# Optimization experiments

Measured on AMD Instinct MI355X. Metric: run time of the kernel, lower is better.

## Reference

```python
import jax, jax.numpy as jnp
import numpy as np

B, N, K = 4, 16384, 32
IN_F, OUT_F = 32, 64


def _dense_params(key, fan_in, fan_out):
    kw, _ = jax.random.split(key)
    lim = np.sqrt(6.0 / (fan_in + fan_out)).astype(np.float32)
    W = jax.random.uniform(kw, (fan_in, fan_out), jnp.float32, -lim, lim)
    b = jnp.zeros((fan_out,), jnp.float32)
    return W, b


def setup_inputs() -> dict:
    key = jax.random.key(0)
    ks = jax.random.split(key, 16)
    points = jax.random.normal(ks[0], (B, N, 3), jnp.float32)
    features = jax.random.normal(ks[1], (B, N, IN_F), jnp.float32)
    density = jax.random.uniform(ks[2], (B, N, 1), jnp.float32)
    neighbor_idx = jax.random.randint(ks[3], (B, N, K), 0, N, jnp.int32)
    pe_w1, pe_b1 = _dense_params(ks[4], 3, 64)
    pe_w2, pe_b2 = _dense_params(ks[5], 64, 64)
    mlp_w1, mlp_b1 = _dense_params(ks[6], IN_F + 64, 128)
    mlp_w2, mlp_b2 = _dense_params(ks[7], 128, OUT_F)
    dw_w1, dw_b1 = _dense_params(ks[8], 1, 64)
    dw_w2, dw_b2 = _dense_params(ks[9], 64, 32)
    dw_w3, dw_b3 = _dense_params(ks[10], 32, 1)
    return dict(points=points, features=features, density=density,
                neighbor_idx=neighbor_idx,
                pe_w1=pe_w1, pe_b1=pe_b1, pe_w2=pe_w2, pe_b2=pe_b2,
                mlp_w1=mlp_w1, mlp_b1=mlp_b1, mlp_w2=mlp_w2, mlp_b2=mlp_b2,
                dw_w1=dw_w1, dw_b1=dw_b1, dw_w2=dw_w2, dw_b2=dw_b2,
                dw_w3=dw_w3, dw_b3=dw_b3)


def _gather(x, idx):
    # x: [B,N,D], idx: [B,N,K] -> [B,N,K,D]
    return jax.vmap(lambda xb, ib: xb[ib])(x, idx)


def reference(points, features, density, neighbor_idx,
              pe_w1, pe_b1, pe_w2, pe_b2,
              mlp_w1, mlp_b1, mlp_w2, mlp_b2,
              dw_w1, dw_b1, dw_w2, dw_b2, dw_w3, dw_b3):
    nb_feat = _gather(features, neighbor_idx)                 # [B,N,K,F]
    rel_pos = _gather(points, neighbor_idx) - points[:, :, None, :]  # [B,N,K,3]
    # positional encoding MLP
    pe = jax.nn.relu(rel_pos @ pe_w1 + pe_b1) @ pe_w2 + pe_b2  # [B,N,K,64]
    cat = jnp.concatenate([nb_feat, pe], axis=-1)              # [B,N,K,F+64]
    h = jax.nn.relu(cat @ mlp_w1 + mlp_b1) @ mlp_w2 + mlp_b2   # [B,N,K,OUT_F]
    # density weight MLP on center density (tiled over K in original)
    cd = density[:, :, None, :]                                # [B,N,1,1]
    w = jax.nn.relu(cd @ dw_w1 + dw_b1)
    w = jax.nn.relu(w @ dw_w2 + dw_b2)
    w = jax.nn.sigmoid(w @ dw_w3 + dw_b3)                      # [B,N,1,1]
    w = jnp.broadcast_to(w, (w.shape[0], w.shape[1], K, 1))    # tile to [B,N,K,1]
    w = jax.nn.softmax(w, axis=2)                              # over neighbors
    return jnp.sum(w * h, axis=2)                              # [B,N,OUT_F]
```

## Files before the change

kernel.cpp:

```cpp
#include <hip/hip_runtime.h>

#define BB   4
#define NN   16384
#define KK   32
#define HID  128
#define OUTF 64

typedef _Float16 f16x8 __attribute__((ext_vector_type(8)));
typedef _Float16 f16x4 __attribute__((ext_vector_type(4)));
typedef _Float16 f16x2 __attribute__((ext_vector_type(2)));
typedef float    f32x4 __attribute__((ext_vector_type(4)));

static __device__ __forceinline__ unsigned short h2u(_Float16 h) {
    union { _Float16 h; unsigned short u; } c; c.h = h; return c.u;
}
static __device__ __forceinline__ _Float16 u2h(unsigned short u) {
    union { _Float16 h; unsigned short u; } c; c.u = u; return c.h;
}

#define PE_HALF(T, RX, RY, RZ)                                              \
    (__builtin_shufflevector((T), (T), 6, 7)                                \
     + __builtin_shufflevector((T), (T), 0, 1) * (RX)                       \
     + __builtin_shufflevector((T), (T), 2, 3) * (RY)                       \
     + __builtin_shufflevector((T), (T), 4, 5) * (RZ))

#define PE_FRAGS(E, O1, O2)                                                 \
    do {                                                                    \
        _Float16 _hx = u2h((E).x), _hy = u2h((E).y), _hz = u2h((E).z);      \
        f16x2 _rx = { _hx, _hx }, _ry = { _hy, _hy }, _rz = { _hz, _hz };   \
        f16x2 _z = { (_Float16)0.f, (_Float16)0.f };                        \
        f16x2 _a0 = __builtin_elementwise_max(PE_HALF(tab1[0], _rx, _ry, _rz), _z); \
        f16x2 _a1 = __builtin_elementwise_max(PE_HALF(tab1[1], _rx, _ry, _rz), _z); \
        f16x2 _a2 = __builtin_elementwise_max(PE_HALF(tab1[2], _rx, _ry, _rz), _z); \
        f16x2 _a3 = __builtin_elementwise_max(PE_HALF(tab1[3], _rx, _ry, _rz), _z); \
        f16x2 _b0 = __builtin_elementwise_max(PE_HALF(tab2[0], _rx, _ry, _rz), _z); \
        f16x2 _b1 = __builtin_elementwise_max(PE_HALF(tab2[1], _rx, _ry, _rz), _z); \
        f16x2 _b2 = __builtin_elementwise_max(PE_HALF(tab2[2], _rx, _ry, _rz), _z); \
        f16x2 _b3 = __builtin_elementwise_max(PE_HALF(tab2[3], _rx, _ry, _rz), _z); \
        f16x4 _al = __builtin_shufflevector(_a0, _a1, 0, 1, 2, 3);          \
        f16x4 _ah = __builtin_shufflevector(_a2, _a3, 0, 1, 2, 3);          \
        f16x4 _bl = __builtin_shufflevector(_b0, _b1, 0, 1, 2, 3);          \
        f16x4 _bh = __builtin_shufflevector(_b2, _b3, 0, 1, 2, 3);          \
        O1 = __builtin_shufflevector(_al, _ah, 0, 1, 2, 3, 4, 5, 6, 7);     \
        O2 = __builtin_shufflevector(_bl, _bh, 0, 1, 2, 3, 4, 5, 6, 7);     \
    } while (0)

__global__ __launch_bounds__(256) void prep_all(
    const float* __restrict__ pe_w2, const float* __restrict__ pe_b2,
    const float* __restrict__ mlp_w1, const float* __restrict__ mlp_b1,
    const float* __restrict__ mlp_w2,
    const float* __restrict__ features, const float* __restrict__ points,
    _Float16* __restrict__ gB1, _Float16* __restrict__ gW2,
    float* __restrict__ b1c,
    _Float16* __restrict__ feat16, float4* __restrict__ pts4)
{
    const int bid = blockIdx.x, tid = threadIdx.x;
    if (bid >= 40) {
        if (bid == 2344) {
            if (tid < HID) {
                float a = mlp_b1[tid];
#pragma unroll 16
                for (int c = 0; c < 64; ++c)
                    a = fmaf(pe_b2[c], mlp_w1[(32 + c) * HID + tid], a);
                b1c[tid] = a;
            }
            return;
        }
        int t = (bid - 40) * 256 + tid;
        if (t < BB * NN * 8) {
            float4 v = ((const float4*)features)[t];
            f16x4 h;
            h[0] = (_Float16)v.x; h[1] = (_Float16)v.y;
            h[2] = (_Float16)v.z; h[3] = (_Float16)v.w;
            *(f16x4*)(feat16 + (size_t)t * 4) = h;
        } else {
            int i = t - BB * NN * 8;
            if (i < BB * NN) {
                const float* p = points + (size_t)i * 3;
                pts4[i] = make_float4(p[0], p[1], p[2], 0.f);
            }
        }
        return;
    }
    if (bid < 24) {
        int ks = bid >> 3, nt = bid & 7;
        for (int e = tid; e < 512; e += 256) {
            int l = e >> 3, j = e & 7;
            int k = ks * 32 + (l >> 4) * 8 + j;
            int n = nt * 16 + (l & 15);
            float v;
            if (k < 32) {
                v = mlp_w1[k * HID + n];
            } else {
                int r = k - 32;
                v = 0.f;
#pragma unroll 16
                for (int c = 0; c < 64; ++c)
                    v = fmaf(pe_w2[r * 64 + c], mlp_w1[(32 + c) * HID + n], v);
            }
            gB1[bid * 512 + e] = (_Float16)v;
        }
    } else {
        int tb = bid - 24;
        int ks = tb >> 2, nt = tb & 3;
        for (int e = tid; e < 512; e += 256) {
            int l = e >> 3, j = e & 7;
            int k = ks * 32 + (l >> 4) * 8 + j;
            int n = nt * 16 + (l & 15);
            gW2[tb * 512 + e] = (_Float16)(mlp_w2[k * OUTF + n] * 0.03125f);
        }
    }
}

__global__ __launch_bounds__(512, 4) void DensityAwareFeatureAggregator_main(
    const float4* __restrict__ pts4,
    const _Float16* __restrict__ feat16,
    const int*   __restrict__ nbr,
    const float* __restrict__ pe_w1,
    const float* __restrict__ pe_b1,
    const float* __restrict__ b1c,
    const _Float16* __restrict__ gB1,
    const _Float16* __restrict__ gW2,
    const float* __restrict__ b2g,
    float* __restrict__ out)
{
    __shared__ __align__(16) _Float16 sB1[24 * 512];
    __shared__ __align__(16) f16x8    sTabH[32];
    __shared__ __align__(16) ushort4  sRI[8][64];
    __shared__ __align__(16) _Float16 sHM[8][16 * 136];

    const int t = threadIdx.x;
    {
        const uint4* g = (const uint4*)gB1;
        uint4* d = (uint4*)sB1;
        for (int i = t; i < 1536; i += 512) d[i] = g[i];
    }
    if (t < 32) {
        int cp = t;
        f16x8 e;
        e[0] = (_Float16)pe_w1[2 * cp];       e[1] = (_Float16)pe_w1[2 * cp + 1];
        e[2] = (_Float16)pe_w1[64 + 2 * cp];  e[3] = (_Float16)pe_w1[64 + 2 * cp + 1];
        e[4] = (_Float16)pe_w1[128 + 2 * cp]; e[5] = (_Float16)pe_w1[128 + 2 * cp + 1];
        e[6] = (_Float16)pe_b1[2 * cp];       e[7] = (_Float16)pe_b1[2 * cp + 1];
        sTabH[cp] = e;
    }
    __syncthreads();

    const int w = t >> 6, l = t & 63, q = l >> 4, c16 = l & 15;
    const int nb   = (blockIdx.x & 7) * 64 + (blockIdx.x >> 3);
    const int base = (nb * 8 + w) * 16;
    const int bo   = base & ~(NN - 1);

    f16x8 tab1[4], tab2[4];
#pragma unroll
    for (int u = 0; u < 4; ++u) {
        tab1[u] = sTabH[q * 4 + u];
        tab2[u] = sTabH[16 + q * 4 + u];
    }
    float bias1[8];
#pragma unroll
    for (int nt = 0; nt < 8; ++nt) bias1[nt] = b1c[nt * 16 + c16];

    const f16x8* B1f = (const f16x8*)sB1;
    _Float16* hmw = &sHM[w][0];

#pragma unroll 1
    for (int p2 = 0; p2 < 8; ++p2) {
        const int mA = base + 2 * p2;
        int idx = nbr[(size_t)mA * KK + l];
        float4 pc = pts4[mA + (l >> 5)];
        float4 pn = pts4[bo + idx];
        ushort4 st;
        st.x = h2u((_Float16)(pn.x - pc.x));
        st.y = h2u((_Float16)(pn.y - pc.y));
        st.z = h2u((_Float16)(pn.z - pc.z));
        st.w = (unsigned short)idx;
        sRI[w][l] = st;
        ushort4 eA0 = sRI[w][c16];
        ushort4 eA1 = sRI[w][16 + c16];
        ushort4 eB0 = sRI[w][32 + c16];
        ushort4 eB1 = sRI[w][48 + c16];

        f16x8 afA0 = ((const f16x8*)(feat16 + ((size_t)(bo + eA0.w)) * 32))[q];
        f16x8 afA1 = ((const f16x8*)(feat16 + ((size_t)(bo + eA1.w)) * 32))[q];
        f16x8 afB0 = ((const f16x8*)(feat16 + ((size_t)(bo + eB0.w)) * 32))[q];
        f16x8 afB1 = ((const f16x8*)(feat16 + ((size_t)(bo + eB1.w)) * 32))[q];

        f16x8 apA10, apA20, apA11, apA21, apB10, apB20, apB11, apB21;
        PE_FRAGS(eA0, apA10, apA20);
        PE_FRAGS(eA1, apA11, apA21);
        PE_FRAGS(eB0, apB10, apB20);
        PE_FRAGS(eB1, apB11, apB21);

#pragma unroll 2
        for (int nt = 0; nt < 8; ++nt) {
            f16x8 bf0 = B1f[nt * 64 + l];
            f16x8 bf1 = B1f[(8 + nt) * 64 + l];
            f16x8 bf2 = B1f[(16 + nt) * 64 + l];
            f32x4 aA0, aA1, aB0, aB1;
            aA0[0] = aA0[1] = aA0[2] = aA0[3] = bias1[nt];
            aA1 = aA0; aB0 = aA0; aB1 = aA0;
            aA0 = __builtin_amdgcn_mfma_f32_16x16x32_f16(afA0,  bf0, aA0, 0, 0, 0);
            aA1 = __builtin_amdgcn_mfma_f32_16x16x32_f16(afA1,  bf0, aA1, 0, 0, 0);
            aB0 = __builtin_amdgcn_mfma_f32_16x16x32_f16(afB0,  bf0, aB0, 0, 0, 0);
            aB1 = __builtin_amdgcn_mfma_f32_16x16x32_f16(afB1,  bf0, aB1, 0, 0, 0);
            aA0 = __builtin_amdgcn_mfma_f32_16x16x32_f16(apA10, bf1, aA0, 0, 0, 0);
            aA1 = __builtin_amdgcn_mfma_f32_16x16x32_f16(apA11, bf1, aA1, 0, 0, 0);
            aB0 = __builtin_amdgcn_mfma_f32_16x16x32_f16(apB10, bf1, aB0, 0, 0, 0);
            aB1 = __builtin_amdgcn_mfma_f32_16x16x32_f16(apB11, bf1, aB1, 0, 0, 0);
            aA0 = __builtin_amdgcn_mfma_f32_16x16x32_f16(apA20, bf2, aA0, 0, 0, 0);
            aA1 = __builtin_amdgcn_mfma_f32_16x16x32_f16(apA21, bf2, aA1, 0, 0, 0);
            aB0 = __builtin_amdgcn_mfma_f32_16x16x32_f16(apB20, bf2, aB0, 0, 0, 0);
            aB1 = __builtin_amdgcn_mfma_f32_16x16x32_f16(apB21, bf2, aB1, 0, 0, 0);

            float sA = fmaxf(aA0[0], 0.f) + fmaxf(aA0[1], 0.f)
                     + fmaxf(aA0[2], 0.f) + fmaxf(aA0[3], 0.f)
                     + fmaxf(aA1[0], 0.f) + fmaxf(aA1[1], 0.f)
                     + fmaxf(aA1[2], 0.f) + fmaxf(aA1[3], 0.f);
            float sB = fmaxf(aB0[0], 0.f) + fmaxf(aB0[1], 0.f)
                     + fmaxf(aB0[2], 0.f) + fmaxf(aB0[3], 0.f)
                     + fmaxf(aB1[0], 0.f) + fmaxf(aB1[1], 0.f)
                     + fmaxf(aB1[2], 0.f) + fmaxf(aB1[3], 0.f);
            sA += __shfl_xor(sA, 16, 64);
            sA += __shfl_xor(sA, 32, 64);
            sB += __shfl_xor(sB, 16, 64);
            sB += __shfl_xor(sB, 32, 64);
            if (q == 0) {
                hmw[(2 * p2) * 136 + nt * 16 + c16]     = (_Float16)sA;
                hmw[(2 * p2 + 1) * 136 + nt * 16 + c16] = (_Float16)sB;
            }
        }
    }

    const f16x8* W2f = (const f16x8*)gW2;
    f32x4 acc2[4];
#pragma unroll
    for (int nt = 0; nt < 4; ++nt) {
        f32x4 z; float bv = b2g[nt * 16 + c16];
        z[0] = z[1] = z[2] = z[3] = bv;
        acc2[nt] = z;
    }
#pragma unroll
    for (int ks = 0; ks < 4; ++ks) {
        f16x8 a2 = *(const f16x8*)&hmw[c16 * 136 + ks * 32 + q * 8];
#pragma unroll
        for (int nt = 0; nt < 4; ++nt) {
            f16x8 bf = W2f[(ks * 4 + nt) * 64 + l];
            acc2[nt] = __builtin_amdgcn_mfma_f32_16x16x32_f16(a2, bf, acc2[nt], 0, 0, 0);
        }
    }
#pragma unroll
    for (int nt = 0; nt < 4; ++nt)
#pragma unroll
        for (int r = 0; r < 4; ++r)
            out[(size_t)(base + q * 4 + r) * OUTF + nt * 16 + c16] = acc2[nt][r];
}

extern "C" void kernel_launch(void* const* d_in, const int* in_sizes, int n_in,
                              void* d_out, int out_size, void* d_ws, size_t ws_size,
                              hipStream_t stream)
{
    const float* points   = (const float*)d_in[0];
    const float* features = (const float*)d_in[1];
    const int*   nbr      = (const int*)d_in[3];
    const float* pe_w1    = (const float*)d_in[4];
    const float* pe_b1    = (const float*)d_in[5];
    const float* pe_w2    = (const float*)d_in[6];
    const float* pe_b2    = (const float*)d_in[7];
    const float* mlp_w1   = (const float*)d_in[8];
    const float* mlp_b1   = (const float*)d_in[9];
    const float* mlp_w2   = (const float*)d_in[10];
    const float* mlp_b2   = (const float*)d_in[11];

    float* wsf = (float*)d_ws;
    float*    b1c    = wsf;
    _Float16* gB1    = (_Float16*)(wsf + 128);
    _Float16* gW2    = (_Float16*)(wsf + 6272);
    float4*   pts4   = (float4*)(wsf + 10368);
    _Float16* feat16 = (_Float16*)(wsf + 272512);

    prep_all<<<2345, 256, 0, stream>>>(
        pe_w2, pe_b2, mlp_w1, mlp_b1, mlp_w2, features, points,
        gB1, gW2, b1c, feat16, pts4);

    DensityAwareFeatureAggregator_main<<<512, 512, 0, stream>>>(
        pts4, feat16, nbr, pe_w1, pe_b1, b1c, gB1, gW2, mlp_b2,
        (float*)d_out);
}
```

Before: 173.8 us.

## Precompute packed fp16 relative positions and indices in prep kernel

Moves the neighbor-index load, point gather and relative-position computation from the main kernel into the prep kernel, which writes a packed ushort4 per (point, neighbor) holding the fp16 offsets and the index. The main kernel then reads these records directly, dropping the per-iteration nbr load, point gathers and the shared-memory round trip through sRI. The cost is an extra 2M-entry buffer written and re-read through global memory, plus a much larger prep grid. The old path is kept as a fallback when the workspace is too small.

```diff
diff --git a/kernel.cpp b/kernel.cpp
--- a/kernel.cpp
+++ b/kernel.cpp
@@ -5,6 +5,10 @@
 #define KK   32
 #define HID  128
 #define OUTF 64
+
+#define PREP_WORK_BLOCKS 10240
+#define PREP_GRID        (40 + PREP_WORK_BLOCKS + 1)
+#define PREP_B1C_BID     (40 + PREP_WORK_BLOCKS)
 
 typedef _Float16 f16x8 __attribute__((ext_vector_type(8)));
 typedef _Float16 f16x4 __attribute__((ext_vector_type(4)));
@@ -45,18 +49,19 @@
         O2 = __builtin_shufflevector(_bl, _bh, 0, 1, 2, 3, 4, 5, 6, 7);     \
     } while (0)
 
-__global__ __launch_bounds__(256) void prep_all(
+__global__ __launch_bounds__(256) void prep_v2(
     const float* __restrict__ pe_w2, const float* __restrict__ pe_b2,
     const float* __restrict__ mlp_w1, const float* __restrict__ mlp_b1,
     const float* __restrict__ mlp_w2,
     const float* __restrict__ features, const float* __restrict__ points,
+    const int* __restrict__ nbr,
     _Float16* __restrict__ gB1, _Float16* __restrict__ gW2,
     float* __restrict__ b1c,
-    _Float16* __restrict__ feat16, float4* __restrict__ pts4)
+    _Float16* __restrict__ feat16, ushort4* __restrict__ rel4)
 {
     const int bid = blockIdx.x, tid = threadIdx.x;
     if (bid >= 40) {
-        if (bid == 2344) {
+        if (bid == PREP_B1C_BID) {
             if (tid < HID) {
                 float a = mlp_b1[tid];
 #pragma unroll 16
@@ -67,17 +72,26 @@
             return;
         }
         int t = (bid - 40) * 256 + tid;
-        if (t < BB * NN * 8) {
-            float4 v = ((const float4*)features)[t];
-            f16x4 h;
-            h[0] = (_Float16)v.x; h[1] = (_Float16)v.y;
-            h[2] = (_Float16)v.z; h[3] = (_Float16)v.w;
-            *(f16x4*)(feat16 + (size_t)t * 4) = h;
+        if (t < BB * NN * KK) {
+            int idx = nbr[t];
+            int pt  = t >> 5;
+            int bo  = pt & ~(NN - 1);
+            const float* pc = points + (size_t)pt * 3;
+            const float* pn = points + (size_t)(bo + idx) * 3;
+            ushort4 st;
+            st.x = h2u((_Float16)(pn[0] - pc[0]));
+            st.y = h2u((_Float16)(pn[1] - pc[1]));
+            st.z = h2u((_Float16)(pn[2] - pc[2]));
+            st.w = (unsigned short)idx;
+            rel4[t] = st;
         } else {
-            int i = t - BB * NN * 8;
-            if (i < BB * NN) {
-                const float* p = points + (size_t)i * 3;
-                pts4[i] = make_float4(p[0], p[1], p[2], 0.f);
+            int u = t - BB * NN * KK;
+            if (u < BB * NN * 8) {
+                float4 v = ((const float4*)features)[u];
+                f16x4 h;
+                h[0] = (_Float16)v.x; h[1] = (_Float16)v.y;
+                h[2] = (_Float16)v.z; h[3] = (_Float16)v.w;
+                *(f16x4*)(feat16 + (size_t)u * 4) = h;
             }
         }
         return;
@@ -113,9 +127,8 @@
 }
 
 __global__ __launch_bounds__(512, 4) void DensityAwareFeatureAggregator_main(
-    const float4* __restrict__ pts4,
+    const ushort4* __restrict__ rel4,
     const _Float16* __restrict__ feat16,
-    const int*   __restrict__ nbr,
     const float* __restrict__ pe_w1,
     const float* __restrict__ pe_b1,
     const float* __restrict__ b1c,
@@ -126,7 +139,6 @@
 {
     __shared__ __align__(16) _Float16 sB1[24 * 512];
     __shared__ __align__(16) f16x8    sTabH[32];
-    __shared__ __align__(16) ushort4  sRI[8][64];
     __shared__ __align__(16) _Float16 sHM[8][16 * 136];
 
     const int t = threadIdx.x;
@@ -167,19 +179,11 @@
 #pragma unroll 1
     for (int p2 = 0; p2 < 8; ++p2) {
         const int mA = base + 2 * p2;
-        int idx = nbr[(size_t)mA * KK + l];
-        float4 pc = pts4[mA + (l >> 5)];
-        float4 pn = pts4[bo + idx];
-        ushort4 st;
-        st.x = h2u((_Float16)(pn.x - pc.x));
-        st.y = h2u((_Float16)(pn.y - pc.y));
-        st.z = h2u((_Float16)(pn.z - pc.z));
-        st.w = (unsigned short)idx;
-        sRI[w][l] = st;
-        ushort4 eA0 = sRI[w][c16];
-        ushort4 eA1 = sRI[w][16 + c16];
-        ushort4 eB0 = sRI[w][32 + c16];
-        ushort4 eB1 = sRI[w][48 + c16];
+        const ushort4* rg = rel4 + (size_t)mA * KK;
+        ushort4 eA0 = rg[c16];
+        ushort4 eA1 = rg[16 + c16];
+        ushort4 eB0 = rg[32 + c16];
+        ushort4 eB1 = rg[48 + c16];
 
         f16x8 afA0 = ((const f16x8*)(feat16 + ((size_t)(bo + eA0.w)) * 32))[q];
         f16x8 afA1 = ((const f16x8*)(feat16 + ((size_t)(bo + eA1.w)) * 32))[q];
@@ -256,6 +260,217 @@
             out[(size_t)(base + q * 4 + r) * OUTF + nt * 16 + c16] = acc2[nt][r];
 }
 
+__global__ __launch_bounds__(256) void prep_fb(
+    const float* __restrict__ pe_w2, const float* __restrict__ pe_b2,
+    const float* __restrict__ mlp_w1, const float* __restrict__ mlp_b1,
+    const float* __restrict__ mlp_w2,
+    const float* __restrict__ features, const float* __restrict__ points,
+    _Float16* __restrict__ gB1, _Float16* __restrict__ gW2,
+    float* __restrict__ b1c,
+    _Float16* __restrict__ feat16, float4* __restrict__ pts4)
+{
+    const int bid = blockIdx.x, tid = threadIdx.x;
+    if (bid >= 40) {
+        if (bid == 2344) {
+            if (tid < HID) {
+                float a = mlp_b1[tid];
+#pragma unroll 16
+                for (int c = 0; c < 64; ++c)
+                    a = fmaf(pe_b2[c], mlp_w1[(32 + c) * HID + tid], a);
+                b1c[tid] = a;
+            }
+            return;
+        }
+        int t = (bid - 40) * 256 + tid;
+        if (t < BB * NN * 8) {
+            float4 v = ((const float4*)features)[t];
+            f16x4 h;
+            h[0] = (_Float16)v.x; h[1] = (_Float16)v.y;
+            h[2] = (_Float16)v.z; h[3] = (_Float16)v.w;
+            *(f16x4*)(feat16 + (size_t)t * 4) = h;
+        } else {
+            int i = t - BB * NN * 8;
+            if (i < BB * NN) {
+                const float* p = points + (size_t)i * 3;
+                pts4[i] = make_float4(p[0], p[1], p[2], 0.f);
+            }
+        }
+        return;
+    }
+    if (bid < 24) {
+        int ks = bid >> 3, nt = bid & 7;
+        for (int e = tid; e < 512; e += 256) {
+            int l = e >> 3, j = e & 7;
+            int k = ks * 32 + (l >> 4) * 8 + j;
+            int n = nt * 16 + (l & 15);
+            float v;
+            if (k < 32) {
+                v = mlp_w1[k * HID + n];
+            } else {
+                int r = k - 32;
+                v = 0.f;
+#pragma unroll 16
+                for (int c = 0; c < 64; ++c)
+                    v = fmaf(pe_w2[r * 64 + c], mlp_w1[(32 + c) * HID + n], v);
+            }
+            gB1[bid * 512 + e] = (_Float16)v;
+        }
+    } else {
+        int tb = bid - 24;
+        int ks = tb >> 2, nt = tb & 3;
+        for (int e = tid; e < 512; e += 256) {
+            int l = e >> 3, j = e & 7;
+            int k = ks * 32 + (l >> 4) * 8 + j;
+            int n = nt * 16 + (l & 15);
+            gW2[tb * 512 + e] = (_Float16)(mlp_w2[k * OUTF + n] * 0.03125f);
+        }
+    }
+}
+
+__global__ __launch_bounds__(512, 4) void main_fb(
+    const float4* __restrict__ pts4,
+    const _Float16* __restrict__ feat16,
+    const int*   __restrict__ nbr,
+    const float* __restrict__ pe_w1,
+    const float* __restrict__ pe_b1,
+    const float* __restrict__ b1c,
+    const _Float16* __restrict__ gB1,
+    const _Float16* __restrict__ gW2,
+    const float* __restrict__ b2g,
+    float* __restrict__ out)
+{
+    __shared__ __align__(16) _Float16 sB1[24 * 512];
+    __shared__ __align__(16) f16x8    sTabH[32];
+    __shared__ __align__(16) ushort4  sRI[8][64];
+    __shared__ __align__(16) _Float16 sHM[8][16 * 136];
+
+    const int t = threadIdx.x;
+    {
+        const uint4* g = (const uint4*)gB1;
+        uint4* d = (uint4*)sB1;
+        for (int i = t; i < 1536; i += 512) d[i] = g[i];
+    }
+    if (t < 32) {
+        int cp = t;
+        f16x8 e;
+        e[0] = (_Float16)pe_w1[2 * cp];       e[1] = (_Float16)pe_w1[2 * cp + 1];
+        e[2] = (_Float16)pe_w1[64 + 2 * cp];  e[3] = (_Float16)pe_w1[64 + 2 * cp + 1];
+        e[4] = (_Float16)pe_w1[128 + 2 * cp]; e[5] = (_Float16)pe_w1[128 + 2 * cp + 1];
+        e[6] = (_Float16)pe_b1[2 * cp];       e[7] = (_Float16)pe_b1[2 * cp + 1];
+        sTabH[cp] = e;
+    }
+    __syncthreads();
+
+    const int w = t >> 6, l = t & 63, q = l >> 4, c16 = l & 15;
+    const int nb   = (blockIdx.x & 7) * 64 + (blockIdx.x >> 3);
+    const int base = (nb * 8 + w) * 16;
+    const int bo   = base & ~(NN - 1);
+
+    f16x8 tab1[4], tab2[4];
+#pragma unroll
+    for (int u = 0; u < 4; ++u) {
+        tab1[u] = sTabH[q * 4 + u];
+        tab2[u] = sTabH[16 + q * 4 + u];
+    }
+    float bias1[8];
+#pragma unroll
+    for (int nt = 0; nt < 8; ++nt) bias1[nt] = b1c[nt * 16 + c16];
+
+    const f16x8* B1f = (const f16x8*)sB1;
+    _Float16* hmw = &sHM[w][0];
+
+#pragma unroll 1
+    for (int p2 = 0; p2 < 8; ++p2) {
+        const int mA = base + 2 * p2;
+        int idx = nbr[(size_t)mA * KK + l];
+        float4 pc = pts4[mA + (l >> 5)];
+        float4 pn = pts4[bo + idx];
+        ushort4 st;
+        st.x = h2u((_Float16)(pn.x - pc.x));
+        st.y = h2u((_Float16)(pn.y - pc.y));
+        st.z = h2u((_Float16)(pn.z - pc.z));
+        st.w = (unsigned short)idx;
+        sRI[w][l] = st;
+        ushort4 eA0 = sRI[w][c16];
+        ushort4 eA1 = sRI[w][16 + c16];
+        ushort4 eB0 = sRI[w][32 + c16];
+        ushort4 eB1 = sRI[w][48 + c16];
+
+        f16x8 afA0 = ((const f16x8*)(feat16 + ((size_t)(bo + eA0.w)) * 32))[q];
+        f16x8 afA1 = ((const f16x8*)(feat16 + ((size_t)(bo + eA1.w)) * 32))[q];
+        f16x8 afB0 = ((const f16x8*)(feat16 + ((size_t)(bo + eB0.w)) * 32))[q];
+        f16x8 afB1 = ((const f16x8*)(feat16 + ((size_t)(bo + eB1.w)) * 32))[q];
+
+        f16x8 apA10, apA20, apA11, apA21, apB10, apB20, apB11, apB21;
+        PE_FRAGS(eA0, apA10, apA20);
+        PE_FRAGS(eA1, apA11, apA21);
+        PE_FRAGS(eB0, apB10, apB20);
+        PE_FRAGS(eB1, apB11, apB21);
+
+#pragma unroll 2
+        for (int nt = 0; nt < 8; ++nt) {
+            f16x8 bf0 = B1f[nt * 64 + l];
+            f16x8 bf1 = B1f[(8 + nt) * 64 + l];
+            f16x8 bf2 = B1f[(16 + nt) * 64 + l];
+            f32x4 aA0, aA1, aB0, aB1;
+            aA0[0] = aA0[1] = aA0[2] = aA0[3] = bias1[nt];
+            aA1 = aA0; aB0 = aA0; aB1 = aA0;
+            aA0 = __builtin_amdgcn_mfma_f32_16x16x32_f16(afA0,  bf0, aA0, 0, 0, 0);
+            aA1 = __builtin_amdgcn_mfma_f32_16x16x32_f16(afA1,  bf0, aA1, 0, 0, 0);
+            aB0 = __builtin_amdgcn_mfma_f32_16x16x32_f16(afB0,  bf0, aB0, 0, 0, 0);
+            aB1 = __builtin_amdgcn_mfma_f32_16x16x32_f16(afB1,  bf0, aB1, 0, 0, 0);
+            aA0 = __builtin_amdgcn_mfma_f32_16x16x32_f16(apA10, bf1, aA0, 0, 0, 0);
+            aA1 = __builtin_amdgcn_mfma_f32_16x16x32_f16(apA11, bf1, aA1, 0, 0, 0);
+            aB0 = __builtin_amdgcn_mfma_f32_16x16x32_f16(apB10, bf1, aB0, 0, 0, 0);
+            aB1 = __builtin_amdgcn_mfma_f32_16x16x32_f16(apB11, bf1, aB1, 0, 0, 0);
+            aA0 = __builtin_amdgcn_mfma_f32_16x16x32_f16(apA20, bf2, aA0, 0, 0, 0);
+            aA1 = __builtin_amdgcn_mfma_f32_16x16x32_f16(apA21, bf2, aA1, 0, 0, 0);
+            aB0 = __builtin_amdgcn_mfma_f32_16x16x32_f16(apB20, bf2, aB0, 0, 0, 0);
+            aB1 = __builtin_amdgcn_mfma_f32_16x16x32_f16(apB21, bf2, aB1, 0, 0, 0);
+
+            float sA = fmaxf(aA0[0], 0.f) + fmaxf(aA0[1], 0.f)
+                     + fmaxf(aA0[2], 0.f) + fmaxf(aA0[3], 0.f)
+                     + fmaxf(aA1[0], 0.f) + fmaxf(aA1[1], 0.f)
+                     + fmaxf(aA1[2], 0.f) + fmaxf(aA1[3], 0.f);
+            float sB = fmaxf(aB0[0], 0.f) + fmaxf(aB0[1], 0.f)
+                     + fmaxf(aB0[2], 0.f) + fmaxf(aB0[3], 0.f)
+                     + fmaxf(aB1[0], 0.f) + fmaxf(aB1[1], 0.f)
+                     + fmaxf(aB1[2], 0.f) + fmaxf(aB1[3], 0.f);
+            sA += __shfl_xor(sA, 16, 64);
+            sA += __shfl_xor(sA, 32, 64);
+            sB += __shfl_xor(sB, 16, 64);
+            sB += __shfl_xor(sB, 32, 64);
+            if (q == 0) {
+                hmw[(2 * p2) * 136 + nt * 16 + c16]     = (_Float16)sA;
+                hmw[(2 * p2 + 1) * 136 + nt * 16 + c16] = (_Float16)sB;
+            }
+        }
+    }
+
+    const f16x8* W2f = (const f16x8*)gW2;
+    f32x4 acc2[4];
+#pragma unroll
+    for (int nt = 0; nt < 4; ++nt) {
+        f32x4 z; float bv = b2g[nt * 16 + c16];
+        z[0] = z[1] = z[2] = z[3] = bv;
+        acc2[nt] = z;
+    }
+#pragma unroll
+    for (int ks = 0; ks < 4; ++ks) {
+        f16x8 a2 = *(const f16x8*)&hmw[c16 * 136 + ks * 32 + q * 8];
+#pragma unroll
+        for (int nt = 0; nt < 4; ++nt) {
+            f16x8 bf = W2f[(ks * 4 + nt) * 64 + l];
+            acc2[nt] = __builtin_amdgcn_mfma_f32_16x16x32_f16(a2, bf, acc2[nt], 0, 0, 0);
+        }
+    }
+#pragma unroll
+    for (int nt = 0; nt < 4; ++nt)
+#pragma unroll
+        for (int r = 0; r < 4; ++r)
+            out[(size_t)(base + q * 4 + r) * OUTF + nt * 16 + c16] = acc2[nt][r];
+}
+
 extern "C" void kernel_launch(void* const* d_in, const int* in_sizes, int n_in,
                               void* d_out, int out_size, void* d_ws, size_t ws_size,
                               hipStream_t stream)
@@ -273,17 +488,35 @@
     const float* mlp_b2   = (const float*)d_in[11];
 
     float* wsf = (float*)d_ws;
-    float*    b1c    = wsf;
-    _Float16* gB1    = (_Float16*)(wsf + 128);
-    _Float16* gW2    = (_Float16*)(wsf + 6272);
-    float4*   pts4   = (float4*)(wsf + 10368);
-    _Float16* feat16 = (_Float16*)(wsf + 272512);
-
-    prep_all<<<2345, 256, 0, stream>>>(
-        pe_w2, pe_b2, mlp_w1, mlp_b1, mlp_w2, features, points,
-        gB1, gW2, b1c, feat16, pts4);
-
-    DensityAwareFeatureAggregator_main<<<512, 512, 0, stream>>>(
-        pts4, feat16, nbr, pe_w1, pe_b1, b1c, gB1, gW2, mlp_b2,
-        (float*)d_out);
-}
+
+    const size_t need_v2 = (size_t)5253248 * 4;
+    if (ws_size >= need_v2) {
+        float*    b1c    = wsf;
+        _Float16* gB1    = (_Float16*)(wsf + 128);
+        _Float16* gW2    = (_Float16*)(wsf + 6272);
+        _Float16* feat16 = (_Float16*)(wsf + 10368);
+        ushort4*  rel4   = (ushort4*)(wsf + 1058944);
+
+        prep_v2<<<PREP_GRID, 256, 0, stream>>>(
+            pe_w2, pe_b2, mlp_w1, mlp_b1, mlp_w2, features, points, nbr,
+            gB1, gW2, b1c, feat16, rel4);
+
+        DensityAwareFeatureAggregator_main<<<512, 512, 0, stream>>>(
+            rel4, feat16, pe_w1, pe_b1, b1c, gB1, gW2, mlp_b2,
+            (float*)d_out);
+    } else {
+        float*    b1c    = wsf;
+        _Float16* gB1    = (_Float16*)(wsf + 128);
+        _Float16* gW2    = (_Float16*)(wsf + 6272);
+        float4*   pts4   = (float4*)(wsf + 10368);
+        _Float16* feat16 = (_Float16*)(wsf + 272512);
+
+        prep_fb<<<2345, 256, 0, stream>>>(
+            pe_w2, pe_b2, mlp_w1, mlp_b1, mlp_w2, features, points,
+            gB1, gW2, b1c, feat16, pts4);
+
+        main_fb<<<512, 512, 0, stream>>>(
+            pts4, feat16, nbr, pe_w1, pe_b1, b1c, gB1, gW2, mlp_b2,
+            (float*)d_out);
+    }
+}
```

Result: slower. 183.0 us (+5.3%).
